# Kernel optimization log

Hardware: AMD Instinct MI355X
Metric: run time of the kernel (lower is better)

The kernel has to match this reference:

```python
import jax, jax.numpy as jnp
import numpy as np

N_NODES = 50000
N_EDGES = 800000
IN_CH = 128
H1, C1 = 8, 16      # conv1: 8 heads x 16 channels, concat -> 128
H2, C2 = 1, 64      # conv2: 1 head x 64 channels, mean (concat=False)
NEG_SLOPE = 0.2


def setup_inputs() -> dict:
    key = jax.random.key(0)
    ks = jax.random.split(key, 10)
    x = jax.random.normal(ks[0], (N_NODES, IN_CH), dtype=jnp.float32)
    edge_index = jax.random.randint(ks[1], (2, N_EDGES), 0, N_NODES, dtype=jnp.int64)
    s1 = 1.0 / np.sqrt(IN_CH)
    s2 = 1.0 / np.sqrt(H1 * C1)
    W1 = jax.random.normal(ks[2], (IN_CH, H1 * C1), dtype=jnp.float32) * s1
    att_src1 = jax.random.normal(ks[3], (H1, C1), dtype=jnp.float32) * s1
    att_dst1 = jax.random.normal(ks[4], (H1, C1), dtype=jnp.float32) * s1
    b1 = jnp.zeros((H1 * C1,), dtype=jnp.float32)
    W2 = jax.random.normal(ks[5], (H1 * C1, H2 * C2), dtype=jnp.float32) * s2
    att_src2 = jax.random.normal(ks[6], (H2, C2), dtype=jnp.float32) * s2
    att_dst2 = jax.random.normal(ks[7], (H2, C2), dtype=jnp.float32) * s2
    b2 = jnp.zeros((C2,), dtype=jnp.float32)
    return {"x": x, "edge_index": edge_index, "W1": W1, "att_src1": att_src1,
            "att_dst1": att_dst1, "b1": b1, "W2": W2, "att_src2": att_src2,
            "att_dst2": att_dst2, "b2": b2}


def gat_conv(x, src, dst, W, att_src, att_dst, bias, heads, out_ch, concat):
    # x: [N, F_in]; src/dst: [E'] (self-loops already appended)
    N = x.shape[0]
    h = (x @ W).reshape(N, heads, out_ch)                     # [N, H, C]
    a_s = jnp.sum(h * att_src[None], axis=-1)                 # [N, H]
    a_d = jnp.sum(h * att_dst[None], axis=-1)                 # [N, H]
    logits = jax.nn.leaky_relu(a_s[src] + a_d[dst], NEG_SLOPE)  # [E', H]
    # segment softmax over edges grouped by destination node
    m = jax.ops.segment_max(logits, dst, num_segments=N)       # [N, H]
    e = jnp.exp(logits - m[dst])                               # [E', H]
    denom = jax.ops.segment_sum(e, dst, num_segments=N)        # [N, H]
    alpha = e / (denom[dst] + 1e-16)                           # [E', H]
    msg = h[src] * alpha[:, :, None]                           # [E', H, C]
    out = jax.ops.segment_sum(msg, dst, num_segments=N)        # [N, H, C]
    if concat:
        out = out.reshape(N, heads * out_ch)
    else:
        out = out.mean(axis=1)
    return out + bias


def reference(x, edge_index, W1, att_src1, att_dst1, b1, W2, att_src2, att_dst2, b2):
    N = x.shape[0]
    loop = jnp.arange(N, dtype=edge_index.dtype)
    src = jnp.concatenate([edge_index[0], loop])   # GATConv adds self-loops
    dst = jnp.concatenate([edge_index[1], loop])
    # eval mode: all dropouts are identity
    h = gat_conv(x, src, dst, W1, att_src1, att_dst1, b1, H1, C1, concat=True)
    h = jax.nn.elu(h)
    out = gat_conv(h, src, dst, W2, att_src2, att_dst2, b2, H2, C2, concat=False)
    return jax.nn.log_softmax(out, axis=1)
```

## Files before the change

### kernel.cpp

```cpp
#include <hip/hip_runtime.h>
#include <math.h>

#define IN_CH 128
#define H1N 8
#define C1N 16
#define C2N 64
#define NEG_SLOPE 0.2f

#define BKT_SHIFT 7
#define BKT_NODES (1 << BKT_SHIFT)
#define NBLK 128

typedef unsigned short ushortT;
typedef short bf16x8 __attribute__((ext_vector_type(8)));
typedef float f32x4 __attribute__((ext_vector_type(4)));

__device__ __forceinline__ ushortT f2bf(float f) {
    unsigned u = __float_as_uint(f);
    unsigned r = u + 0x7FFFu + ((u >> 16) & 1u);
    return (ushortT)(r >> 16);
}
__device__ __forceinline__ float bf2f(ushortT b) {
    return __uint_as_float(((unsigned)b) << 16);
}
__device__ __forceinline__ float leaky(float x) {
    return (x > 0.f) ? x : NEG_SLOPE * x;
}


__global__ __launch_bounds__(512) void k_cnt(const int* __restrict__ src,
                                             const int* __restrict__ dst,
                                             int E, int N, int* __restrict__ cnt) {
    __shared__ int hist[512];
    int blk = blockIdx.x, t = threadIdx.x;
    int nb = (N + BKT_NODES - 1) >> BKT_SHIFT;
    if (t < nb) hist[t] = 0;
    __syncthreads();
    int Etot = E + N;
    int chunk = (Etot + gridDim.x - 1) / gridDim.x;
    int lo = blk * chunk;
    int hi = lo + chunk; if (hi > Etot) hi = Etot;
    for (int i = lo + t; i < hi; i += 512) {
        int d = (i < E) ? dst[i] : (i - E);
        atomicAdd(&hist[d >> BKT_SHIFT], 1);
    }
    __syncthreads();
    if (t < nb) cnt[t * NBLK + blk] = hist[t];
}

__global__ __launch_bounds__(NBLK) void k_scanrel(int* __restrict__ cnt,
                                                  int* __restrict__ bucketTotal) {
    __shared__ int sh[NBLK];
    int b = blockIdx.x, t = threadIdx.x;
    sh[t] = cnt[b * NBLK + t];
    __syncthreads();
    for (int off = 1; off < NBLK; off <<= 1) {
        int v = (t >= off) ? sh[t - off] : 0;
        __syncthreads();
        sh[t] += v;
        __syncthreads();
    }
    if (t == NBLK - 1) bucketTotal[b] = sh[t];
    cnt[b * NBLK + t] = (t == 0) ? 0 : sh[t - 1];
}

__global__ __launch_bounds__(512) void k_scanbucket(const int* __restrict__ bucketTotal,
                                                    int nb, int* __restrict__ bBase,
                                                    int N, int* __restrict__ offsets) {
    __shared__ int sh[512];
    int t = threadIdx.x;
    sh[t] = (t < nb) ? bucketTotal[t] : 0;
    __syncthreads();
    for (int off = 1; off < 512; off <<= 1) {
        int v = (t >= off) ? sh[t - off] : 0;
        __syncthreads();
        sh[t] += v;
        __syncthreads();
    }
    if (t < nb) bBase[t] = (t == 0) ? 0 : sh[t - 1];
    if (t == 511) { bBase[nb] = sh[511]; offsets[N] = sh[511]; }
}

__global__ __launch_bounds__(512) void k_bin(const int* __restrict__ src,
                                             const int* __restrict__ dst,
                                             int E, int N,
                                             const int* __restrict__ cnt,
                                             const int* __restrict__ bBase,
                                             unsigned* __restrict__ pair) {
    __shared__ int cur[512];
    int blk = blockIdx.x, t = threadIdx.x;
    int nb = (N + BKT_NODES - 1) >> BKT_SHIFT;
    if (t < nb) cur[t] = bBase[t] + cnt[t * NBLK + blk];
    __syncthreads();
    int Etot = E + N;
    int chunk = (Etot + gridDim.x - 1) / gridDim.x;
    int lo = blk * chunk;
    int hi = lo + chunk; if (hi > Etot) hi = Etot;
    for (int i = lo + t; i < hi; i += 512) {
        int s, d;
        if (i < E) { s = src[i]; d = dst[i]; }
        else       { s = d = i - E; }
        int b = d >> BKT_SHIFT;
        int pos = atomicAdd(&cur[b], 1);
        pair[pos] = ((unsigned)(d & (BKT_NODES - 1)) << 16) | (unsigned)s;
    }
}

__global__ __launch_bounds__(256) void k_csr_local(const unsigned* __restrict__ pair,
                                                   const int* __restrict__ bBase,
                                                   int N, int* __restrict__ offsets,
                                                   ushortT* __restrict__ csr) {
    __shared__ int hist[BKT_NODES];
    __shared__ int loff[BKT_NODES];
    int b = blockIdx.x;
    int t = threadIdx.x;
    int base = bBase[b];
    int cnt = bBase[b + 1] - base;
    const unsigned* pp = pair + base;

    if (t < BKT_NODES) hist[t] = 0;
    __syncthreads();
    for (int i = t; i < cnt; i += 256) atomicAdd(&hist[pp[i] >> 16], 1);
    __syncthreads();
    if (t < BKT_NODES) loff[t] = hist[t];
    __syncthreads();
    for (int off = 1; off < BKT_NODES; off <<= 1) {
        int v = 0;
        if (t < BKT_NODES && t >= off) v = loff[t - off];
        __syncthreads();
        if (t < BKT_NODES) loff[t] += v;
        __syncthreads();
    }
    int node0 = b << BKT_SHIFT;
    if (t < BKT_NODES) {
        int excl = (t == 0) ? 0 : loff[t - 1];
        hist[t] = excl;
        int g = node0 + t;
        if (g < N) offsets[g] = base + excl;
    }
    __syncthreads();
    for (int i = t; i < cnt; i += 256) {
        unsigned pk = pp[i];
        int pos = atomicAdd(&hist[pk >> 16], 1);
        csr[base + pos] = (ushortT)(pk & 0xFFFFu);
    }
}


template <int KOUT, int HEADS, bool BFIN>
__global__ __launch_bounds__(256) void k_gemm_att(const void* __restrict__ Av,
                                                  const float* __restrict__ W,
                                                  const float* __restrict__ att_s,
                                                  const float* __restrict__ att_d,
                                                  int N, ushortT* __restrict__ Cbf,
                                                  float* __restrict__ as_,
                                                  float* __restrict__ ad_) {
    constexpr int NT = KOUT / 16;
    constexpr int LDK = IN_CH + 8;
    __shared__ ushortT Alds[64][LDK];
    __shared__ ushortT Wlds[KOUT][LDK];
    int t = threadIdx.x;
    int row0 = blockIdx.x * 64;
    int w    = t >> 6;
    int lane = t & 63;
    int lm   = lane & 15;
    int lg   = lane >> 4;

    for (int idx = t; idx < 64 * 32; idx += 256) {
        int r  = idx >> 5;
        int c4 = (idx & 31) << 2;
        int gr = row0 + r;
        ushort4 u; u.x = 0; u.y = 0; u.z = 0; u.w = 0;
        if (gr < N) {
            if constexpr (BFIN) {
                u = *(const ushort4*)((const ushortT*)Av + (size_t)gr * IN_CH + c4);
            } else {
                float4 v = *(const float4*)((const float*)Av + (size_t)gr * IN_CH + c4);
                u.x = f2bf(v.x); u.y = f2bf(v.y); u.z = f2bf(v.z); u.w = f2bf(v.w);
            }
        }
        *(ushort4*)(&Alds[r][c4]) = u;
    }
    for (int idx = t; idx < IN_CH * KOUT; idx += 256) {
        int k = idx / KOUT;
        int n = idx % KOUT;
        Wlds[n][k] = f2bf(W[(size_t)k * KOUT + n]);
    }
    __syncthreads();

    f32x4 acc[NT];
#pragma unroll
    for (int ct = 0; ct < NT; ++ct) acc[ct] = (f32x4){0.f, 0.f, 0.f, 0.f};

    int ar = w * 16 + lm;
#pragma unroll
    for (int ks = 0; ks < 4; ++ks) {
        int kb = ks * 32 + lg * 8;
        bf16x8 af = *(const bf16x8*)(&Alds[ar][kb]);
#pragma unroll
        for (int ct = 0; ct < NT; ++ct) {
            bf16x8 bf = *(const bf16x8*)(&Wlds[ct * 16 + lm][kb]);
            acc[ct] = __builtin_amdgcn_mfma_f32_16x16x32_bf16(af, bf, acc[ct], 0, 0, 0);
        }
    }

    float asp0 = 0.f, asp1 = 0.f, asp2 = 0.f, asp3 = 0.f;
    float adp0 = 0.f, adp1 = 0.f, adp2 = 0.f, adp3 = 0.f;
#pragma unroll
    for (int ct = 0; ct < NT; ++ct) {
        int gcol = ct * 16 + lm;
        float sc = att_s[gcol];
        float dc = att_d[gcol];
        float c0 = acc[ct][0], c1 = acc[ct][1], c2 = acc[ct][2], c3 = acc[ct][3];
#pragma unroll
        for (int i = 0; i < 4; ++i) {
            int gr = row0 + w * 16 + lg * 4 + i;
            if (gr < N) Cbf[(size_t)gr * KOUT + gcol] = f2bf(acc[ct][i]);
        }
        if constexpr (HEADS == 1) {
            asp0 = fmaf(c0, sc, asp0); asp1 = fmaf(c1, sc, asp1);
            asp2 = fmaf(c2, sc, asp2); asp3 = fmaf(c3, sc, asp3);
            adp0 = fmaf(c0, dc, adp0); adp1 = fmaf(c1, dc, adp1);
            adp2 = fmaf(c2, dc, adp2); adp3 = fmaf(c3, dc, adp3);
        } else {
            float r0 = c0 * sc, r1 = c1 * sc, r2 = c2 * sc, r3 = c3 * sc;
            float q0 = c0 * dc, q1 = c1 * dc, q2 = c2 * dc, q3 = c3 * dc;
#pragma unroll
            for (int off = 1; off < 16; off <<= 1) {
                r0 += __shfl_xor(r0, off); r1 += __shfl_xor(r1, off);
                r2 += __shfl_xor(r2, off); r3 += __shfl_xor(r3, off);
                q0 += __shfl_xor(q0, off); q1 += __shfl_xor(q1, off);
                q2 += __shfl_xor(q2, off); q3 += __shfl_xor(q3, off);
            }
            if (lm == 0) {
                int grb = row0 + w * 16 + lg * 4;
                if (grb + 0 < N) { as_[(size_t)(grb + 0) * HEADS + ct] = r0; ad_[(size_t)(grb + 0) * HEADS + ct] = q0; }
                if (grb + 1 < N) { as_[(size_t)(grb + 1) * HEADS + ct] = r1; ad_[(size_t)(grb + 1) * HEADS + ct] = q1; }
                if (grb + 2 < N) { as_[(size_t)(grb + 2) * HEADS + ct] = r2; ad_[(size_t)(grb + 2) * HEADS + ct] = q2; }
                if (grb + 3 < N) { as_[(size_t)(grb + 3) * HEADS + ct] = r3; ad_[(size_t)(grb + 3) * HEADS + ct] = q3; }
            }
        }
    }
    if constexpr (HEADS == 1) {
#pragma unroll
        for (int off = 1; off < 16; off <<= 1) {
            asp0 += __shfl_xor(asp0, off); asp1 += __shfl_xor(asp1, off);
            asp2 += __shfl_xor(asp2, off); asp3 += __shfl_xor(asp3, off);
            adp0 += __shfl_xor(adp0, off); adp1 += __shfl_xor(adp1, off);
            adp2 += __shfl_xor(adp2, off); adp3 += __shfl_xor(adp3, off);
        }
        if (lm == 0) {
            int grb = row0 + w * 16 + lg * 4;
            if (grb + 0 < N) { as_[grb + 0] = asp0; ad_[grb + 0] = adp0; }
            if (grb + 1 < N) { as_[grb + 1] = asp1; ad_[grb + 1] = adp1; }
            if (grb + 2 < N) { as_[grb + 2] = asp2; ad_[grb + 2] = adp2; }
            if (grb + 3 < N) { as_[grb + 3] = asp3; ad_[grb + 3] = adp3; }
        }
    }
}


__global__ void k_agg1(const ushortT* __restrict__ h1bf,
                       const float* __restrict__ as1, const float* __restrict__ ad1,
                       const int* __restrict__ offsets, const ushortT* __restrict__ csr,
                       const float* __restrict__ b1,
                       int N, ushortT* __restrict__ h2in) {
    int wid  = (blockIdx.x * blockDim.x + threadIdx.x) >> 6;
    int lane = threadIdx.x & 63;
    if (wid >= N) return;
    int v = wid;
    int hc = lane >> 3;
    int hp = lane & 7;
    float adc = ad1[v * H1N + hc];
    float adp = ad1[v * H1N + hp];
    float denom = 0.f, acc0 = 0.f, acc1 = 0.f;
    int beg = offsets[v], end = offsets[v + 1];
    int j = beg;
    for (; j + 8 <= end; j += 8) {
        int ep = lane >> 3;
        int sE = csr[j + ep];
        float a = as1[sE * H1N + hp];
        float pp = __expf(leaky(a + adp));
#pragma unroll
        for (int e = 0; e < 8; ++e) {
            int srcl = e * 8 + hc;
            float pe = __shfl(pp, srcl);
            int   se = __shfl(sE, srcl);
            unsigned q = *(const unsigned*)(h1bf + (size_t)se * IN_CH + lane * 2);
            denom += pe;
            acc0 = fmaf(pe, bf2f((ushortT)(q & 0xFFFFu)), acc0);
            acc1 = fmaf(pe, bf2f((ushortT)(q >> 16)), acc1);
        }
    }
    if (j + 4 <= end) {
        int ep = (lane >> 3) & 3;
        int sE = csr[j + ep];
        float a = as1[sE * H1N + hp];
        float pp = __expf(leaky(a + adp));
#pragma unroll
        for (int e = 0; e < 4; ++e) {
            int srcl = e * 8 + hc;
            float pe = __shfl(pp, srcl);
            int   se = __shfl(sE, srcl);
            unsigned q = *(const unsigned*)(h1bf + (size_t)se * IN_CH + lane * 2);
            denom += pe;
            acc0 = fmaf(pe, bf2f((ushortT)(q & 0xFFFFu)), acc0);
            acc1 = fmaf(pe, bf2f((ushortT)(q >> 16)), acc1);
        }
        j += 4;
    }
    for (; j < end; ++j) {
        int s = csr[j];
        float a = as1[s * H1N + hc];
        unsigned q = *(const unsigned*)(h1bf + (size_t)s * IN_CH + lane * 2);
        float p = __expf(leaky(a + adc));
        denom += p;
        acc0 = fmaf(p, bf2f((ushortT)(q & 0xFFFFu)), acc0);
        acc1 = fmaf(p, bf2f((ushortT)(q >> 16)), acc1);
    }
    float inv = 1.f / (denom + 1e-16f);
    float o0 = acc0 * inv + b1[lane * 2];
    float o1 = acc1 * inv + b1[lane * 2 + 1];
    o0 = (o0 > 0.f) ? o0 : expm1f(o0);
    o1 = (o1 > 0.f) ? o1 : expm1f(o1);
    unsigned pk = ((unsigned)f2bf(o1) << 16) | (unsigned)f2bf(o0);
    *(unsigned*)(h2in + (size_t)v * IN_CH + lane * 2) = pk;
}


__global__ __launch_bounds__(256) void k_agg2(const ushortT* __restrict__ h2bf,
                       const float* __restrict__ as2, const float* __restrict__ ad2,
                       const int* __restrict__ offsets, const ushortT* __restrict__ csr,
                       const float* __restrict__ b2,
                       int N, float* __restrict__ out) {
    int wid  = (blockIdx.x * blockDim.x + threadIdx.x) >> 6;
    int lane = threadIdx.x & 63;
    int half = lane >> 5;
    int v = wid * 2 + half;
    bool alive = (v < N);
    int c2 = (lane & 31) * 2;

    float ad = 0.f;
    int beg = 0, end = 0;
    if (alive) {
        ad = ad2[v];
        beg = offsets[v];
        end = offsets[v + 1];
    }
    float denom = 0.f, acc0 = 0.f, acc1 = 0.f;
    int j = beg;
    for (; j + 8 <= end; j += 8) {
        int sE = csr[j + (lane & 7)];
        float p = __expf(leaky(as2[sE] + ad));
#pragma unroll
        for (int e = 0; e < 8; ++e) {
            int srcl = (lane & 32) + e;
            float pe = __shfl(p, srcl);
            int   se = __shfl(sE, srcl);
            unsigned q = *(const unsigned*)(h2bf + (size_t)se * C2N + c2);
            denom += pe;
            acc0 = fmaf(pe, bf2f((ushortT)(q & 0xFFFFu)), acc0);
            acc1 = fmaf(pe, bf2f((ushortT)(q >> 16)), acc1);
        }
    }
    if (j < end) {
        int m = end - j;
        int ep = lane & 7;
        int sE = 0;
        float p = 0.f;
        if (ep < m) {
            sE = csr[j + ep];
            p = __expf(leaky(as2[sE] + ad));
        }
        for (int e = 0; e < m; ++e) {
            int srcl = (lane & 32) + e;
            float pe = __shfl(p, srcl);
            int   se = __shfl(sE, srcl);
            unsigned q = *(const unsigned*)(h2bf + (size_t)se * C2N + c2);
            denom += pe;
            acc0 = fmaf(pe, bf2f((ushortT)(q & 0xFFFFu)), acc0);
            acc1 = fmaf(pe, bf2f((ushortT)(q >> 16)), acc1);
        }
    }
    float inv = 1.f / (denom + 1e-16f);
    float o0 = acc0 * inv + b2[c2];
    float o1 = acc1 * inv + b2[c2 + 1];
    float mx = fmaxf(o0, o1);
#pragma unroll
    for (int off = 16; off >= 1; off >>= 1) mx = fmaxf(mx, __shfl_xor(mx, off));
    float se2 = __expf(o0 - mx) + __expf(o1 - mx);
#pragma unroll
    for (int off = 16; off >= 1; off >>= 1) se2 += __shfl_xor(se2, off);
    if (alive) {
        float lse = logf(se2);
        float2 ov; ov.x = o0 - mx - lse; ov.y = o1 - mx - lse;
        *(float2*)(out + (size_t)v * C2N + c2) = ov;
    }
}


extern "C" void kernel_launch(void* const* d_in, const int* in_sizes, int n_in,
                              void* d_out, int out_size, void* d_ws, size_t ws_size,
                              hipStream_t stream) {
    const float* x      = (const float*)d_in[0];
    const int*   ei     = (const int*)d_in[1];
    const float* W1     = (const float*)d_in[2];
    const float* att_s1 = (const float*)d_in[3];
    const float* att_d1 = (const float*)d_in[4];
    const float* b1     = (const float*)d_in[5];
    const float* W2     = (const float*)d_in[6];
    const float* att_s2 = (const float*)d_in[7];
    const float* att_d2 = (const float*)d_in[8];
    const float* b2     = (const float*)d_in[9];

    int N = in_sizes[0] / IN_CH;
    int E = in_sizes[1] / 2;
    const int* srcA = ei;
    const int* dstA = ei + E;
    int Etot = E + N;
    int nb = (N + BKT_NODES - 1) >> BKT_SHIFT;

    char* p = (char*)d_ws;
    auto carve = [&](size_t bytes) {
        void* r = (void*)p;
        p += (bytes + 255) & ~(size_t)255;
        return r;
    };
    ushortT* h1bf = (ushortT*)carve((size_t)N * IN_CH * 2);
    ushortT* h2bf = (ushortT*)carve((size_t)N * C2N * 2);
    ushortT* h2in = (ushortT*)carve((size_t)N * IN_CH * 2);
    float* as1  = (float*)carve((size_t)N * H1N * 4);
    float* ad1  = (float*)carve((size_t)N * H1N * 4);
    float* as2  = (float*)carve((size_t)N * 4);
    float* ad2  = (float*)carve((size_t)N * 4);
    int* offsets     = (int*)carve((size_t)(N + 1) * 4);
    ushortT* csr     = (ushortT*)carve((size_t)(Etot + 32) * 2);
    int* cnt         = (int*)carve((size_t)nb * NBLK * 4);
    int* bucketTotal = (int*)carve((size_t)nb * 4);
    int* bBase       = (int*)carve((size_t)(nb + 1) * 4);
    unsigned* pair   = (unsigned*)carve((size_t)Etot * 4);

    k_cnt<<<NBLK, 512, 0, stream>>>(srcA, dstA, E, N, cnt);
    k_scanrel<<<nb, NBLK, 0, stream>>>(cnt, bucketTotal);
    k_scanbucket<<<1, 512, 0, stream>>>(bucketTotal, nb, bBase, N, offsets);
    k_bin<<<NBLK, 512, 0, stream>>>(srcA, dstA, E, N, cnt, bBase, pair);
    k_csr_local<<<nb, 256, 0, stream>>>(pair, bBase, N, offsets, csr);

    k_gemm_att<128, 8, false><<<(N + 63) / 64, 256, 0, stream>>>(x, W1, att_s1, att_d1,
                                                                 N, h1bf, as1, ad1);
    k_agg1<<<(N * 64 + 255) / 256, 256, 0, stream>>>(h1bf, as1, ad1, offsets, csr, b1, N, h2in);

    k_gemm_att<64, 1, true><<<(N + 63) / 64, 256, 0, stream>>>(h2in, W2, att_s2, att_d2,
                                                               N, h2bf, as2, ad2);
    k_agg2<<<(N * 32 + 255) / 256, 256, 0, stream>>>(h2bf, as2, ad2, offsets, csr, b2,
                                                     N, (float*)d_out);
}
```

Measured before the change: 138.2 us.

## Pre-cast weights to transposed bf16 once and double GEMM row tile

Adds a small kernel that converts W1 and W2 to transposed bf16 a single time, so each GEMM block stops re-reading fp32 W with a strided transpose and per-element conversion. Each block now covers 128 rows instead of 64, with every wave computing two 16-row subtiles, which spreads the W staging cost over twice as many rows. The bf16 input tile load is widened to 8-element vectors. The price is two extra launches, more LDS per block and fewer blocks, which may lower occupancy.

```diff
diff --git a/kernel.cpp b/kernel.cpp
--- a/kernel.cpp
+++ b/kernel.cpp
@@ -14,6 +14,7 @@
 typedef unsigned short ushortT;
 typedef short bf16x8 __attribute__((ext_vector_type(8)));
 typedef float f32x4 __attribute__((ext_vector_type(4)));
+typedef ushortT us8 __attribute__((ext_vector_type(8)));
 
 __device__ __forceinline__ ushortT f2bf(float f) {
     unsigned u = __float_as_uint(f);
@@ -147,9 +148,19 @@
 }
 
 
+__global__ void k_wcast(const float* __restrict__ W, int K, int KOUT,
+                        ushortT* __restrict__ Wt) {
+    int id = blockIdx.x * blockDim.x + threadIdx.x;
+    if (id < K * KOUT) {
+        int n = id / K, k = id % K;
+        Wt[id] = f2bf(W[(size_t)k * KOUT + n]);
+    }
+}
+
+
 template <int KOUT, int HEADS, bool BFIN>
 __global__ __launch_bounds__(256) void k_gemm_att(const void* __restrict__ Av,
-                                                  const float* __restrict__ W,
+                                                  const ushortT* __restrict__ Wt,
                                                   const float* __restrict__ att_s,
                                                   const float* __restrict__ att_d,
                                                   int N, ushortT* __restrict__ Cbf,
@@ -157,104 +168,119 @@
                                                   float* __restrict__ ad_) {
     constexpr int NT = KOUT / 16;
     constexpr int LDK = IN_CH + 8;
-    __shared__ ushortT Alds[64][LDK];
+    __shared__ ushortT Alds[128][LDK];
     __shared__ ushortT Wlds[KOUT][LDK];
     int t = threadIdx.x;
-    int row0 = blockIdx.x * 64;
+    int row0 = blockIdx.x * 128;
     int w    = t >> 6;
     int lane = t & 63;
     int lm   = lane & 15;
     int lg   = lane >> 4;
 
-    for (int idx = t; idx < 64 * 32; idx += 256) {
-        int r  = idx >> 5;
-        int c4 = (idx & 31) << 2;
-        int gr = row0 + r;
-        ushort4 u; u.x = 0; u.y = 0; u.z = 0; u.w = 0;
-        if (gr < N) {
-            if constexpr (BFIN) {
-                u = *(const ushort4*)((const ushortT*)Av + (size_t)gr * IN_CH + c4);
-            } else {
+    if constexpr (BFIN) {
+        for (int idx = t; idx < 128 * 16; idx += 256) {
+            int r  = idx >> 4;
+            int c8 = (idx & 15) << 3;
+            int gr = row0 + r;
+            us8 u = (us8){0,0,0,0,0,0,0,0};
+            if (gr < N) u = *(const us8*)((const ushortT*)Av + (size_t)gr * IN_CH + c8);
+            *(us8*)(&Alds[r][c8]) = u;
+        }
+    } else {
+        for (int idx = t; idx < 128 * 32; idx += 256) {
+            int r  = idx >> 5;
+            int c4 = (idx & 31) << 2;
+            int gr = row0 + r;
+            ushort4 u; u.x = 0; u.y = 0; u.z = 0; u.w = 0;
+            if (gr < N) {
                 float4 v = *(const float4*)((const float*)Av + (size_t)gr * IN_CH + c4);
                 u.x = f2bf(v.x); u.y = f2bf(v.y); u.z = f2bf(v.z); u.w = f2bf(v.w);
             }
-        }
-        *(ushort4*)(&Alds[r][c4]) = u;
-    }
-    for (int idx = t; idx < IN_CH * KOUT; idx += 256) {
-        int k = idx / KOUT;
-        int n = idx % KOUT;
-        Wlds[n][k] = f2bf(W[(size_t)k * KOUT + n]);
-    }
-    __syncthreads();
-
-    f32x4 acc[NT];
-#pragma unroll
-    for (int ct = 0; ct < NT; ++ct) acc[ct] = (f32x4){0.f, 0.f, 0.f, 0.f};
-
-    int ar = w * 16 + lm;
-#pragma unroll
-    for (int ks = 0; ks < 4; ++ks) {
-        int kb = ks * 32 + lg * 8;
-        bf16x8 af = *(const bf16x8*)(&Alds[ar][kb]);
+            *(ushort4*)(&Alds[r][c4]) = u;
+        }
+    }
+    for (int idx = t; idx < KOUT * 16; idx += 256) {
+        int n  = idx >> 4;
+        int kb = (idx & 15) << 3;
+        *(us8*)(&Wlds[n][kb]) = *(const us8*)(Wt + (size_t)n * IN_CH + kb);
+    }
+    __syncthreads();
+
+    f32x4 acc[2][NT];
+#pragma unroll
+    for (int s = 0; s < 2; ++s)
+#pragma unroll
+        for (int ct = 0; ct < NT; ++ct) acc[s][ct] = (f32x4){0.f, 0.f, 0.f, 0.f};
+
+#pragma unroll
+    for (int s = 0; s < 2; ++s) {
+        int ar = w * 32 + s * 16 + lm;
+#pragma unroll
+        for (int ks = 0; ks < 4; ++ks) {
+            int kb = ks * 32 + lg * 8;
+            bf16x8 af = *(const bf16x8*)(&Alds[ar][kb]);
+#pragma unroll
+            for (int ct = 0; ct < NT; ++ct) {
+                bf16x8 bf = *(const bf16x8*)(&Wlds[ct * 16 + lm][kb]);
+                acc[s][ct] = __builtin_amdgcn_mfma_f32_16x16x32_bf16(af, bf, acc[s][ct], 0, 0, 0);
+            }
+        }
+    }
+
+#pragma unroll
+    for (int s = 0; s < 2; ++s) {
+        int rb = row0 + w * 32 + s * 16 + lg * 4;
+        float asp0 = 0.f, asp1 = 0.f, asp2 = 0.f, asp3 = 0.f;
+        float adp0 = 0.f, adp1 = 0.f, adp2 = 0.f, adp3 = 0.f;
 #pragma unroll
         for (int ct = 0; ct < NT; ++ct) {
-            bf16x8 bf = *(const bf16x8*)(&Wlds[ct * 16 + lm][kb]);
-            acc[ct] = __builtin_amdgcn_mfma_f32_16x16x32_bf16(af, bf, acc[ct], 0, 0, 0);
-        }
-    }
-
-    float asp0 = 0.f, asp1 = 0.f, asp2 = 0.f, asp3 = 0.f;
-    float adp0 = 0.f, adp1 = 0.f, adp2 = 0.f, adp3 = 0.f;
-#pragma unroll
-    for (int ct = 0; ct < NT; ++ct) {
-        int gcol = ct * 16 + lm;
-        float sc = att_s[gcol];
-        float dc = att_d[gcol];
-        float c0 = acc[ct][0], c1 = acc[ct][1], c2 = acc[ct][2], c3 = acc[ct][3];
-#pragma unroll
-        for (int i = 0; i < 4; ++i) {
-            int gr = row0 + w * 16 + lg * 4 + i;
-            if (gr < N) Cbf[(size_t)gr * KOUT + gcol] = f2bf(acc[ct][i]);
+            int gcol = ct * 16 + lm;
+            float sc = att_s[gcol];
+            float dc = att_d[gcol];
+            float c0 = acc[s][ct][0], c1 = acc[s][ct][1];
+            float c2 = acc[s][ct][2], c3 = acc[s][ct][3];
+#pragma unroll
+            for (int i = 0; i < 4; ++i) {
+                int gr = rb + i;
+                if (gr < N) Cbf[(size_t)gr * KOUT + gcol] = f2bf(acc[s][ct][i]);
+            }
+            if constexpr (HEADS == 1) {
+                asp0 = fmaf(c0, sc, asp0); asp1 = fmaf(c1, sc, asp1);
+                asp2 = fmaf(c2, sc, asp2); asp3 = fmaf(c3, sc, asp3);
+                adp0 = fmaf(c0, dc, adp0); adp1 = fmaf(c1, dc, adp1);
+                adp2 = fmaf(c2, dc, adp2); adp3 = fmaf(c3, dc, adp3);
+            } else {
+                float r0 = c0 * sc, r1 = c1 * sc, r2 = c2 * sc, r3 = c3 * sc;
+                float q0 = c0 * dc, q1 = c1 * dc, q2 = c2 * dc, q3 = c3 * dc;
+#pragma unroll
+                for (int off = 1; off < 16; off <<= 1) {
+                    r0 += __shfl_xor(r0, off); r1 += __shfl_xor(r1, off);
+                    r2 += __shfl_xor(r2, off); r3 += __shfl_xor(r3, off);
+                    q0 += __shfl_xor(q0, off); q1 += __shfl_xor(q1, off);
+                    q2 += __shfl_xor(q2, off); q3 += __shfl_xor(q3, off);
+                }
+                if (lm == 0) {
+                    if (rb + 0 < N) { as_[(size_t)(rb + 0) * HEADS + ct] = r0; ad_[(size_t)(rb + 0) * HEADS + ct] = q0; }
+                    if (rb + 1 < N) { as_[(size_t)(rb + 1) * HEADS + ct] = r1; ad_[(size_t)(rb + 1) * HEADS + ct] = q1; }
+                    if (rb + 2 < N) { as_[(size_t)(rb + 2) * HEADS + ct] = r2; ad_[(size_t)(rb + 2) * HEADS + ct] = q2; }
+                    if (rb + 3 < N) { as_[(size_t)(rb + 3) * HEADS + ct] = r3; ad_[(size_t)(rb + 3) * HEADS + ct] = q3; }
+                }
+            }
         }
         if constexpr (HEADS == 1) {
-            asp0 = fmaf(c0, sc, asp0); asp1 = fmaf(c1, sc, asp1);
-            asp2 = fmaf(c2, sc, asp2); asp3 = fmaf(c3, sc, asp3);
-            adp0 = fmaf(c0, dc, adp0); adp1 = fmaf(c1, dc, adp1);
-            adp2 = fmaf(c2, dc, adp2); adp3 = fmaf(c3, dc, adp3);
-        } else {
-            float r0 = c0 * sc, r1 = c1 * sc, r2 = c2 * sc, r3 = c3 * sc;
-            float q0 = c0 * dc, q1 = c1 * dc, q2 = c2 * dc, q3 = c3 * dc;
 #pragma unroll
             for (int off = 1; off < 16; off <<= 1) {
-                r0 += __shfl_xor(r0, off); r1 += __shfl_xor(r1, off);
-                r2 += __shfl_xor(r2, off); r3 += __shfl_xor(r3, off);
-                q0 += __shfl_xor(q0, off); q1 += __shfl_xor(q1, off);
-                q2 += __shfl_xor(q2, off); q3 += __shfl_xor(q3, off);
+                asp0 += __shfl_xor(asp0, off); asp1 += __shfl_xor(asp1, off);
+                asp2 += __shfl_xor(asp2, off); asp3 += __shfl_xor(asp3, off);
+                adp0 += __shfl_xor(adp0, off); adp1 += __shfl_xor(adp1, off);
+                adp2 += __shfl_xor(adp2, off); adp3 += __shfl_xor(adp3, off);
             }
             if (lm == 0) {
-                int grb = row0 + w * 16 + lg * 4;
-                if (grb + 0 < N) { as_[(size_t)(grb + 0) * HEADS + ct] = r0; ad_[(size_t)(grb + 0) * HEADS + ct] = q0; }
-                if (grb + 1 < N) { as_[(size_t)(grb + 1) * HEADS + ct] = r1; ad_[(size_t)(grb + 1) * HEADS + ct] = q1; }
-                if (grb + 2 < N) { as_[(size_t)(grb + 2) * HEADS + ct] = r2; ad_[(size_t)(grb + 2) * HEADS + ct] = q2; }
-                if (grb + 3 < N) { as_[(size_t)(grb + 3) * HEADS + ct] = r3; ad_[(size_t)(grb + 3) * HEADS + ct] = q3; }
-            }
-        }
-    }
-    if constexpr (HEADS == 1) {
-#pragma unroll
-        for (int off = 1; off < 16; off <<= 1) {
-            asp0 += __shfl_xor(asp0, off); asp1 += __shfl_xor(asp1, off);
-            asp2 += __shfl_xor(asp2, off); asp3 += __shfl_xor(asp3, off);
-            adp0 += __shfl_xor(adp0, off); adp1 += __shfl_xor(adp1, off);
-            adp2 += __shfl_xor(adp2, off); adp3 += __shfl_xor(adp3, off);
-        }
-        if (lm == 0) {
-            int grb = row0 + w * 16 + lg * 4;
-            if (grb + 0 < N) { as_[grb + 0] = asp0; ad_[grb + 0] = adp0; }
-            if (grb + 1 < N) { as_[grb + 1] = asp1; ad_[grb + 1] = adp1; }
-            if (grb + 2 < N) { as_[grb + 2] = asp2; ad_[grb + 2] = adp2; }
-            if (grb + 3 < N) { as_[grb + 3] = asp3; ad_[grb + 3] = adp3; }
+                if (rb + 0 < N) { as_[rb + 0] = asp0; ad_[rb + 0] = adp0; }
+                if (rb + 1 < N) { as_[rb + 1] = asp1; ad_[rb + 1] = adp1; }
+                if (rb + 2 < N) { as_[rb + 2] = asp2; ad_[rb + 2] = adp2; }
+                if (rb + 3 < N) { as_[rb + 3] = asp3; ad_[rb + 3] = adp3; }
+            }
         }
     }
 }
@@ -439,6 +465,11 @@
     int* bucketTotal = (int*)carve((size_t)nb * 4);
     int* bBase       = (int*)carve((size_t)(nb + 1) * 4);
     unsigned* pair   = (unsigned*)carve((size_t)Etot * 4);
+    ushortT* W1t     = (ushortT*)carve((size_t)IN_CH * IN_CH * 2);
+    ushortT* W2t     = (ushortT*)carve((size_t)IN_CH * C2N * 2);
+
+    k_wcast<<<(IN_CH * IN_CH + 255) / 256, 256, 0, stream>>>(W1, IN_CH, IN_CH, W1t);
+    k_wcast<<<(IN_CH * C2N + 255) / 256, 256, 0, stream>>>(W2, IN_CH, C2N, W2t);
 
     k_cnt<<<NBLK, 512, 0, stream>>>(srcA, dstA, E, N, cnt);
     k_scanrel<<<nb, NBLK, 0, stream>>>(cnt, bucketTotal);
@@ -446,12 +477,12 @@
     k_bin<<<NBLK, 512, 0, stream>>>(srcA, dstA, E, N, cnt, bBase, pair);
     k_csr_local<<<nb, 256, 0, stream>>>(pair, bBase, N, offsets, csr);
 
-    k_gemm_att<128, 8, false><<<(N + 63) / 64, 256, 0, stream>>>(x, W1, att_s1, att_d1,
-                                                                 N, h1bf, as1, ad1);
+    k_gemm_att<128, 8, false><<<(N + 127) / 128, 256, 0, stream>>>(x, W1t, att_s1, att_d1,
+                                                                   N, h1bf, as1, ad1);
     k_agg1<<<(N * 64 + 255) / 256, 256, 0, stream>>>(h1bf, as1, ad1, offsets, csr, b1, N, h2in);
 
-    k_gemm_att<64, 1, true><<<(N + 63) / 64, 256, 0, stream>>>(h2in, W2, att_s2, att_d2,
-                                                               N, h2bf, as2, ad2);
+    k_gemm_att<64, 1, true><<<(N + 127) / 128, 256, 0, stream>>>(h2in, W2t, att_s2, att_d2,
+                                                                 N, h2bf, as2, ad2);
     k_agg2<<<(N * 32 + 255) / 256, 256, 0, stream>>>(h2bf, as2, ad2, offsets, csr, b2,
                                                      N, (float*)d_out);
 }
```

Result: no change. 140.1 us (+1.4%).
